# Kernel optimization log

Hardware: AMD Instinct MI355X
Metric: run time of the kernel (lower is better)

The kernel has to match this reference:

```python
import jax, jax.numpy as jnp
import numpy as np

EMPHASIS_FACTOR = 1.5

def setup_inputs() -> dict:
    key = jax.random.key(0)
    k1, k2 = jax.random.split(key)
    B, T, F = 32, 4096, 256
    x = jax.random.normal(k1, (B, T, F), dtype=jnp.float32)
    W = jax.random.normal(k2, (F, 1), dtype=jnp.float32) * (1.0 / np.sqrt(F))
    b = jnp.zeros((1,), dtype=jnp.float32)
    return {"x": x, "W": W, "b": b}

def reference(x, W, b):
    # x: [B, T, F], W: [F, 1], b: [1]
    B, T, F = x.shape
    e = jnp.tanh(x @ W + b)                 # [B, T, 1]
    a = jax.nn.softmax(e, axis=1)           # softmax over time
    a_flat = a[..., 0]                      # [B, T]
    k = max(1, int(T * 0.1))
    _, top_idx = jax.lax.top_k(a_flat, k)   # [B, k]
    # scatter True at top-k positions (instead of O(T*k) broadcast compare)
    mask = jnp.zeros((B, T), dtype=bool).at[jnp.arange(B)[:, None], top_idx].set(True)
    a_emph = jnp.where(mask[..., None], a * EMPHASIS_FACTOR, a)  # [B, T, 1]
    return jnp.sum(x * a_emph, axis=1, keepdims=True)            # [B, 1, F]
```

## Files before the change

### kernel.cpp

```cpp
#include <hip/hip_runtime.h>
#include <math.h>

#define BB 32
#define TT 4096
#define FF 256
#define CH 64
#define NC (TT / CH)
#define ST 16
#define K_TOP 409
#define NSEG 16
#define SEGT (TT / NSEG)
#define CPS (NC / NSEG)

__device__ __forceinline__ unsigned flip_key(float v) {
    unsigned u = __float_as_uint(v);
    return (u & 0x80000000u) ? ~u : (u | 0x80000000u);
}

__global__ void zero_kernel(float* __restrict__ p, int n) {
    int i = blockIdx.x * 256 + threadIdx.x;
    if (i < n) p[i] = 0.f;
}

__global__ __launch_bounds__(256) void fused_pass1(const float* __restrict__ x,
                                                   const float* __restrict__ W,
                                                   const float* __restrict__ bias,
                                                   float* __restrict__ e,
                                                   float* __restrict__ P,
                                                   float* __restrict__ cm,
                                                   float* __restrict__ cs) {
    const int b = blockIdx.x / NC;
    const int c = blockIdx.x % NC;
    const int tid = threadIdx.x;
    const int wv = tid >> 6, ln = tid & 63;

    const float* xc = x + ((size_t)b * TT + (size_t)c * CH) * FF;
    const float4 wvec = ((const float4*)W)[ln];
    const float  bb   = bias[0];

    __shared__ float se[ST];
    __shared__ float4 part4[4][64];
    __shared__ float swsum[4];

    float4 acc = make_float4(0.f, 0.f, 0.f, 0.f);
    float  m = -1e30f, ssum = 0.f;

    for (int s0 = 0; s0 < CH; s0 += ST) {
        float4 xr[4];
        #pragma unroll
        for (int i = 0; i < 4; i++) {
            const int tl = s0 + wv * 4 + i;
            xr[i] = ((const float4*)(xc + (size_t)tl * FF))[ln];
        }
        float dv[4];
        #pragma unroll
        for (int i = 0; i < 4; i++)
            dv[i] = xr[i].x * wvec.x + xr[i].y * wvec.y +
                    xr[i].z * wvec.z + xr[i].w * wvec.w;
        #pragma unroll
        for (int i = 0; i < 4; i++) {
            float d = dv[i];
            #pragma unroll
            for (int off = 32; off; off >>= 1) d += __shfl_xor(d, off);
            dv[i] = tanhf(d + bb);
        }
        __syncthreads();
        if (ln == 0) {
            #pragma unroll
            for (int i = 0; i < 4; i++) {
                se[wv * 4 + i] = dv[i];
                e[(size_t)b * TT + c * CH + s0 + wv * 4 + i] = dv[i];
            }
        }
        __syncthreads();

        float lm = m;
        #pragma unroll
        for (int i = 0; i < ST; i++) lm = fmaxf(lm, se[i]);
        const float alpha = __expf(m - lm);
        acc.x *= alpha; acc.y *= alpha; acc.z *= alpha; acc.w *= alpha;
        ssum *= alpha;
        #pragma unroll
        for (int i = 0; i < 4; i++) {
            const float wgt = __expf(dv[i] - lm);
            ssum += wgt;
            acc.x += wgt * xr[i].x; acc.y += wgt * xr[i].y;
            acc.z += wgt * xr[i].z; acc.w += wgt * xr[i].w;
        }
        m = lm;
    }

    part4[wv][ln] = acc;
    if (ln == 0) swsum[wv] = ssum;
    __syncthreads();
    const float* pf = (const float*)part4;
    const float p = pf[tid] + pf[256 + tid] + pf[512 + tid] + pf[768 + tid];
    P[((size_t)b * NC + c) * FF + tid] = p;
    if (tid == 0) {
        cm[b * NC + c] = m;
        cs[b * NC + c] = swsum[0] + swsum[1] + swsum[2] + swsum[3];
    }
}

__global__ __launch_bounds__(256) void select_kernel(const float* __restrict__ e,
                                                     const float* __restrict__ cm,
                                                     const float* __restrict__ cs,
                                                     float* __restrict__ stats) {
    const int b = blockIdx.x;
    const int tid = threadIdx.x;
    const int wv = tid >> 6, ln = tid & 63;

    __shared__ float sgm, sZ;
    __shared__ int sc[4];

    if (tid < 64) {
        const float mm = cm[b * NC + tid];
        const float ss = cs[b * NC + tid];
        float g = mm;
        #pragma unroll
        for (int off = 32; off; off >>= 1) g = fmaxf(g, __shfl_xor(g, off));
        float zz = ss * __expf(mm - g);
        #pragma unroll
        for (int off = 32; off; off >>= 1) zz += __shfl_xor(zz, off);
        if (tid == 0) { sgm = g; sZ = zz; }
    }

    const float* eb = e + (size_t)b * TT;
    unsigned key[16];
    #pragma unroll
    for (int j = 0; j < 16; j++) key[j] = flip_key(eb[tid + 256 * j]);

    unsigned prefix = 0u, mask = 0u;
    int kk = K_TOP;
    for (int bit = 31; bit >= 0; bit--) {
        const unsigned bm = 1u << bit;
        const unsigned m2 = mask | bm;
        const unsigned want = prefix | bm;
        int cnt = 0;
        #pragma unroll
        for (int j = 0; j < 16; j++) cnt += (int)((key[j] & m2) == want);
        #pragma unroll
        for (int off = 32; off; off >>= 1) cnt += __shfl_down(cnt, off);
        __syncthreads();
        if (ln == 0) sc[wv] = cnt;
        __syncthreads();
        const int tot = sc[0] + sc[1] + sc[2] + sc[3];
        if (tot >= kk) prefix = want; else kk -= tot;
        mask = m2;
    }

    if (tid == 0) {
        stats[3 * b + 0] = sgm;
        stats[3 * b + 1] = sZ;
        stats[3 * b + 2] = __uint_as_float(prefix);
    }
}

__global__ __launch_bounds__(256) void combine_kernel(const float* __restrict__ x,
                                                      const float* __restrict__ e,
                                                      const float* __restrict__ P,
                                                      const float* __restrict__ cm,
                                                      const float* __restrict__ stats,
                                                      float* __restrict__ out) {
    const int b = blockIdx.x / NSEG;
    const int s = blockIdx.x % NSEG;
    const int tid = threadIdx.x;

    const float gmax = stats[3 * b + 0];
    const float Z    = stats[3 * b + 1];
    const unsigned Kkey = __float_as_uint(stats[3 * b + 2]);

    float acc = 0.f;
    #pragma unroll
    for (int c = 0; c < CPS; c++) {
        const int cc = s * CPS + c;
        const float sc2 = __expf(cm[b * NC + cc] - gmax);
        acc += P[((size_t)b * NC + cc) * FF + tid] * sc2;
    }

    __shared__ int scount;
    __shared__ int slist[SEGT];
    __shared__ float sval[SEGT];
    if (tid == 0) scount = 0;
    __syncthreads();

    const int t = s * SEGT + tid;
    const float ev = e[(size_t)b * TT + t];
    if (flip_key(ev) >= Kkey) {
        const int i = atomicAdd(&scount, 1);
        slist[i] = t;
        sval[i] = ev;
    }
    __syncthreads();

    const int n = scount;
    for (int i = 0; i < n; i++) {
        const float coeff = 0.5f * __expf(sval[i] - gmax);
        acc += coeff * x[((size_t)b * TT + slist[i]) * FF + tid];
    }

    atomicAdd(&out[b * FF + tid], acc / Z);
}

extern "C" void kernel_launch(void* const* d_in, const int* in_sizes, int n_in,
                              void* d_out, int out_size, void* d_ws, size_t ws_size,
                              hipStream_t stream) {
    const float* x    = (const float*)d_in[0];
    const float* W    = (const float*)d_in[1];
    const float* bias = (const float*)d_in[2];
    float* out = (float*)d_out;

    float* e     = (float*)d_ws;
    float* P     = e + (size_t)BB * TT;
    float* cm    = P + (size_t)BB * NC * FF;
    float* cs    = cm + BB * NC;
    float* stats = cs + BB * NC;

    zero_kernel<<<(BB * FF + 255) / 256, 256, 0, stream>>>(out, BB * FF);
    fused_pass1<<<BB * NC, 256, 0, stream>>>(x, W, bias, e, P, cm, cs);
    select_kernel<<<BB, 256, 0, stream>>>(e, cm, cs, stats);
    combine_kernel<<<BB * NSEG, 256, 0, stream>>>(x, e, P, cm, stats, out);
}
```

Measured before the change: 217.9 us.

## Remove pass1 block syncs, fuse select and combine, use fast tanh and ballot counting

Pass1 now keeps a per-wave online softmax max and rescales the wave partials at the end, removing the two block-wide barriers and the shared staging per 16-row step. tanhf is replaced by an exp/rcp approximation. The radix select counts matches with ballot+popcount instead of shuffle reductions. Select and combine are merged into a single per-batch kernel that writes the output directly, dropping the zero kernel and output atomics. The fused kernel runs on only 32 blocks and gathers selected rows serially, which reduces parallelism in that stage.

```diff
diff --git a/kernel.cpp b/kernel.cpp
--- a/kernel.cpp
+++ b/kernel.cpp
@@ -6,20 +6,21 @@
 #define FF 256
 #define CH 64
 #define NC (TT / CH)
-#define ST 16
 #define K_TOP 409
-#define NSEG 16
-#define SEGT (TT / NSEG)
-#define CPS (NC / NSEG)
+#define EMPH_HALF 0.5f
 
 __device__ __forceinline__ unsigned flip_key(float v) {
     unsigned u = __float_as_uint(v);
     return (u & 0x80000000u) ? ~u : (u | 0x80000000u);
 }
-
-__global__ void zero_kernel(float* __restrict__ p, int n) {
-    int i = blockIdx.x * 256 + threadIdx.x;
-    if (i < n) p[i] = 0.f;
+__device__ __forceinline__ float unflip_key(unsigned k) {
+    unsigned u = (k & 0x80000000u) ? (k & 0x7fffffffu) : ~k;
+    return __uint_as_float(u);
+}
+__device__ __forceinline__ float fast_tanh(float z) {
+    z = fminf(fmaxf(z, -15.f), 15.f);
+    const float t = __expf(2.f * z);
+    return (t - 1.f) * __builtin_amdgcn_rcpf(t + 1.f);
 }
 
 __global__ __launch_bounds__(256) void fused_pass1(const float* __restrict__ x,
@@ -38,20 +39,17 @@
     const float4 wvec = ((const float4*)W)[ln];
     const float  bb   = bias[0];
 
-    __shared__ float se[ST];
-    __shared__ float4 part4[4][64];
-    __shared__ float swsum[4];
-
     float4 acc = make_float4(0.f, 0.f, 0.f, 0.f);
     float  m = -1e30f, ssum = 0.f;
 
-    for (int s0 = 0; s0 < CH; s0 += ST) {
+    #pragma unroll
+    for (int s0 = 0; s0 < CH; s0 += 16) {
+        const int r0 = s0 + wv * 4;
         float4 xr[4];
         #pragma unroll
-        for (int i = 0; i < 4; i++) {
-            const int tl = s0 + wv * 4 + i;
-            xr[i] = ((const float4*)(xc + (size_t)tl * FF))[ln];
-        }
+        for (int i = 0; i < 4; i++)
+            xr[i] = ((const float4*)(xc + (size_t)(r0 + i) * FF))[ln];
+
         float dv[4];
         #pragma unroll
         for (int i = 0; i < 4; i++)
@@ -62,21 +60,15 @@
             float d = dv[i];
             #pragma unroll
             for (int off = 32; off; off >>= 1) d += __shfl_xor(d, off);
-            dv[i] = tanhf(d + bb);
+            dv[i] = fast_tanh(d + bb);
         }
-        __syncthreads();
-        if (ln == 0) {
-            #pragma unroll
-            for (int i = 0; i < 4; i++) {
-                se[wv * 4 + i] = dv[i];
-                e[(size_t)b * TT + c * CH + s0 + wv * 4 + i] = dv[i];
-            }
-        }
-        __syncthreads();
+        if (ln == 0)
+            *(float4*)(e + (size_t)b * TT + c * CH + r0) =
+                make_float4(dv[0], dv[1], dv[2], dv[3]);
 
         float lm = m;
         #pragma unroll
-        for (int i = 0; i < ST; i++) lm = fmaxf(lm, se[i]);
+        for (int i = 0; i < 4; i++) lm = fmaxf(lm, dv[i]);
         const float alpha = __expf(m - lm);
         acc.x *= alpha; acc.y *= alpha; acc.z *= alpha; acc.w *= alpha;
         ssum *= alpha;
@@ -90,28 +82,42 @@
         m = lm;
     }
 
+    __shared__ float4 part4[4][64];
+    __shared__ float sm[4], ss4[4];
     part4[wv][ln] = acc;
-    if (ln == 0) swsum[wv] = ssum;
-    __syncthreads();
+    if (ln == 0) { sm[wv] = m; ss4[wv] = ssum; }
+    __syncthreads();
+
+    const float m0 = sm[0], m1 = sm[1], m2 = sm[2], m3 = sm[3];
+    const float mc = fmaxf(fmaxf(m0, m1), fmaxf(m2, m3));
+    const float s0s = __expf(m0 - mc), s1s = __expf(m1 - mc);
+    const float s2s = __expf(m2 - mc), s3s = __expf(m3 - mc);
     const float* pf = (const float*)part4;
-    const float p = pf[tid] + pf[256 + tid] + pf[512 + tid] + pf[768 + tid];
+    const float p = pf[tid] * s0s + pf[256 + tid] * s1s +
+                    pf[512 + tid] * s2s + pf[768 + tid] * s3s;
     P[((size_t)b * NC + c) * FF + tid] = p;
     if (tid == 0) {
-        cm[b * NC + c] = m;
-        cs[b * NC + c] = swsum[0] + swsum[1] + swsum[2] + swsum[3];
-    }
-}
-
-__global__ __launch_bounds__(256) void select_kernel(const float* __restrict__ e,
-                                                     const float* __restrict__ cm,
-                                                     const float* __restrict__ cs,
-                                                     float* __restrict__ stats) {
+        cm[b * NC + c] = mc;
+        cs[b * NC + c] = ss4[0] * s0s + ss4[1] * s1s + ss4[2] * s2s + ss4[3] * s3s;
+    }
+}
+
+__global__ __launch_bounds__(256) void select_combine(const float* __restrict__ x,
+                                                      const float* __restrict__ e,
+                                                      const float* __restrict__ P,
+                                                      const float* __restrict__ cm,
+                                                      const float* __restrict__ cs,
+                                                      float* __restrict__ out) {
     const int b = blockIdx.x;
     const int tid = threadIdx.x;
     const int wv = tid >> 6, ln = tid & 63;
 
     __shared__ float sgm, sZ;
-    __shared__ int sc[4];
+    __shared__ int   sc4[4];
+    __shared__ float sscale[NC];
+    __shared__ int   scount;
+    __shared__ int   slist[TT];
+    __shared__ float sval[TT];
 
     if (tid < 64) {
         const float mm = cm[b * NC + tid];
@@ -122,13 +128,15 @@
         float zz = ss * __expf(mm - g);
         #pragma unroll
         for (int off = 32; off; off >>= 1) zz += __shfl_xor(zz, off);
-        if (tid == 0) { sgm = g; sZ = zz; }
+        if (tid == 0) { sgm = g; sZ = zz; scount = 0; }
     }
 
     const float* eb = e + (size_t)b * TT;
     unsigned key[16];
     #pragma unroll
     for (int j = 0; j < 16; j++) key[j] = flip_key(eb[tid + 256 * j]);
+    __syncthreads();
+    if (tid < 64) sscale[tid] = __expf(cm[b * NC + tid] - sgm);
 
     unsigned prefix = 0u, mask = 0u;
     int kk = K_TOP;
@@ -138,68 +146,41 @@
         const unsigned want = prefix | bm;
         int cnt = 0;
         #pragma unroll
-        for (int j = 0; j < 16; j++) cnt += (int)((key[j] & m2) == want);
-        #pragma unroll
-        for (int off = 32; off; off >>= 1) cnt += __shfl_down(cnt, off);
+        for (int j = 0; j < 16; j++)
+            cnt += (int)__popcll(__ballot((key[j] & m2) == want));
         __syncthreads();
-        if (ln == 0) sc[wv] = cnt;
+        if (ln == 0) sc4[wv] = cnt;
         __syncthreads();
-        const int tot = sc[0] + sc[1] + sc[2] + sc[3];
+        const int tot = sc4[0] + sc4[1] + sc4[2] + sc4[3];
         if (tot >= kk) prefix = want; else kk -= tot;
         mask = m2;
     }
-
-    if (tid == 0) {
-        stats[3 * b + 0] = sgm;
-        stats[3 * b + 1] = sZ;
-        stats[3 * b + 2] = __uint_as_float(prefix);
-    }
-}
-
-__global__ __launch_bounds__(256) void combine_kernel(const float* __restrict__ x,
-                                                      const float* __restrict__ e,
-                                                      const float* __restrict__ P,
-                                                      const float* __restrict__ cm,
-                                                      const float* __restrict__ stats,
-                                                      float* __restrict__ out) {
-    const int b = blockIdx.x / NSEG;
-    const int s = blockIdx.x % NSEG;
-    const int tid = threadIdx.x;
-
-    const float gmax = stats[3 * b + 0];
-    const float Z    = stats[3 * b + 1];
-    const unsigned Kkey = __float_as_uint(stats[3 * b + 2]);
+    const unsigned Kkey = prefix;
 
     float acc = 0.f;
+    #pragma unroll 4
+    for (int c = 0; c < NC; c++)
+        acc += P[((size_t)b * NC + c) * FF + tid] * sscale[c];
+
     #pragma unroll
-    for (int c = 0; c < CPS; c++) {
-        const int cc = s * CPS + c;
-        const float sc2 = __expf(cm[b * NC + cc] - gmax);
-        acc += P[((size_t)b * NC + cc) * FF + tid] * sc2;
-    }
-
-    __shared__ int scount;
-    __shared__ int slist[SEGT];
-    __shared__ float sval[SEGT];
-    if (tid == 0) scount = 0;
-    __syncthreads();
-
-    const int t = s * SEGT + tid;
-    const float ev = e[(size_t)b * TT + t];
-    if (flip_key(ev) >= Kkey) {
-        const int i = atomicAdd(&scount, 1);
-        slist[i] = t;
-        sval[i] = ev;
-    }
-    __syncthreads();
-
+    for (int j = 0; j < 16; j++) {
+        if (key[j] >= Kkey) {
+            const int i = atomicAdd(&scount, 1);
+            slist[i] = tid + 256 * j;
+            sval[i]  = unflip_key(key[j]);
+        }
+    }
+    __syncthreads();
     const int n = scount;
-    for (int i = 0; i < n; i++) {
-        const float coeff = 0.5f * __expf(sval[i] - gmax);
-        acc += coeff * x[((size_t)b * TT + slist[i]) * FF + tid];
-    }
-
-    atomicAdd(&out[b * FF + tid], acc / Z);
+    for (int i = tid; i < n; i += 256)
+        sval[i] = EMPH_HALF * __expf(sval[i] - sgm);
+    __syncthreads();
+
+    const float* xb = x + (size_t)b * TT * FF;
+    for (int i = 0; i < n; i++)
+        acc += sval[i] * xb[(size_t)slist[i] * FF + tid];
+
+    out[b * FF + tid] = acc * (1.f / sZ);
 }
 
 extern "C" void kernel_launch(void* const* d_in, const int* in_sizes, int n_in,
@@ -214,10 +195,7 @@
     float* P     = e + (size_t)BB * TT;
     float* cm    = P + (size_t)BB * NC * FF;
     float* cs    = cm + BB * NC;
-    float* stats = cs + BB * NC;
-
-    zero_kernel<<<(BB * FF + 255) / 256, 256, 0, stream>>>(out, BB * FF);
+
     fused_pass1<<<BB * NC, 256, 0, stream>>>(x, W, bias, e, P, cm, cs);
-    select_kernel<<<BB, 256, 0, stream>>>(e, cm, cs, stats);
-    combine_kernel<<<BB * NSEG, 256, 0, stream>>>(x, e, P, cm, stats, out);
-}
+    select_combine<<<BB, 256, 0, stream>>>(x, e, P, cm, cs, out);
+}
```

New measurement: 231.0 us. +6.0%, slower.
